# Performance work log

Measured on AMD Instinct MI355X. Metric: run time of the kernel, lower is better.

The kernel has to match this reference:

```python
import jax, jax.numpy as jnp
import numpy as np

NUM_HEADS = 4
GROUPS = 8
EPS = 1e-5


def setup_inputs() -> dict:
    key = jax.random.key(0)
    ks = jax.random.split(key, 8)
    B, C, H, W = 8, 512, 64, 64
    L, E = 77, 768
    std = 0.02
    return {
        "x": jax.random.normal(ks[0], (B, C, H, W), jnp.float32),
        "text_emb": jax.random.normal(ks[1], (B, L, E), jnp.float32),
        "attention_mask": jax.random.randint(ks[2], (B, L), 0, 2, jnp.int32),
        "Wq_w": jax.random.normal(ks[3], (C, C), jnp.float32) * std,
        "Wq_b": jnp.zeros((C,), jnp.float32),
        "Wk_w": jax.random.normal(ks[4], (C, E), jnp.float32) * std,
        "Wk_b": jnp.zeros((C,), jnp.float32),
        "Wv_w": jax.random.normal(ks[5], (C, E), jnp.float32) * std,
        "Wv_b": jnp.zeros((C,), jnp.float32),
        "gn_scale": jnp.ones((C,), jnp.float32),
        "gn_bias": jnp.zeros((C,), jnp.float32),
    }


def reference(x, text_emb, attention_mask, Wq_w, Wq_b, Wk_w, Wk_b, Wv_w, Wv_b, gn_scale, gn_bias):
    B, C, H, W = x.shape
    dh = C // NUM_HEADS
    scale = dh ** -0.5

    # [B, HW, C] queries from image features
    x_flat = x.reshape(B, C, H * W).transpose(0, 2, 1)
    Q = x_flat @ Wq_w.T + Wq_b                 # [B, S, C]
    K = text_emb @ Wk_w.T + Wk_b               # [B, L, C]
    V = text_emb @ Wv_w.T + Wv_b               # [B, L, C]

    def split_heads(t):
        Bt, T, _ = t.shape
        return t.reshape(Bt, T, NUM_HEADS, dh).transpose(0, 2, 1, 3)  # [B, h, T, dh]

    Qh, Kh, Vh = split_heads(Q), split_heads(K), split_heads(V)

    scores = jnp.einsum("bhqd,bhkd->bhqk", Qh, Kh) * scale  # [B, h, S, L]
    mask = (attention_mask == 0)[:, None, None, :]
    scores = jnp.where(mask, -jnp.inf, scores)
    probs = jax.nn.softmax(scores, axis=-1)
    # dropout layers are identity in eval mode
    attn = jnp.einsum("bhqk,bhkd->bhqd", probs, Vh)          # [B, h, S, dh]

    out = attn.transpose(0, 2, 1, 3).reshape(B, H * W, C)    # [B, S, C]
    out = out.transpose(0, 2, 1).reshape(B, C, H, W)

    # GroupNorm(8 groups, affine) over (C/G, H, W) per group
    g = out.reshape(B, GROUPS, -1)
    mean = g.mean(axis=-1, keepdims=True)
    var = g.var(axis=-1, keepdims=True)
    g = (g - mean) * jax.lax.rsqrt(var + EPS)
    out = g.reshape(B, C, H, W) * gn_scale[None, :, None, None] + gn_bias[None, :, None, None]
    return out
```

## Files before the change

### kernel.cpp

```cpp
#include <hip/hip_runtime.h>
#include <hip/hip_bf16.h>
#include <cstdint>


typedef __attribute__((ext_vector_type(8))) short short8;
typedef __attribute__((ext_vector_type(4))) short short4v;
typedef __attribute__((ext_vector_type(4))) float f32x4;

#define DEV __device__ __forceinline__

DEV float bf2f(unsigned short u){ union{uint32_t i; float f;} x; x.i = ((uint32_t)u) << 16; return x.f; }
DEV unsigned short f2bf(float f){ __hip_bfloat16 h = __float2bfloat16(f); return *reinterpret_cast<unsigned short*>(&h); }
DEV short8 ld8(const unsigned short* p){ return *reinterpret_cast<const short8*>(p); }
DEV f32x4 ldf4(const float* p){ return *reinterpret_cast<const f32x4*>(p); }

#if defined(__has_builtin)
#if __has_builtin(__builtin_amdgcn_global_load_lds)
#define HAVE_ASYNC_LDS 1
#endif
#endif

__global__ __launch_bounds__(256) void k_fat(const float* __restrict__ x,
                                             unsigned short* __restrict__ xTt,
                                             const float* __restrict__ text,
                                             const float* __restrict__ Wk,
                                             const float* __restrict__ Wkb,
                                             const float* __restrict__ Wv,
                                             const float* __restrict__ Wvb,
                                             unsigned short* __restrict__ wsK,
                                             unsigned short* __restrict__ wsVt,
                                             const float* __restrict__ Wq,
                                             unsigned short* __restrict__ wsWqT,
                                             int b0, int s_base, int slen, int SB){
  __shared__ unsigned short U[16896];
  const int tid = threadIdx.x;
  const int bx = blockIdx.x, by = blockIdx.y, bz = blockIdx.z;
  const int bg = b0 + bz;

  if (bx >= 3){
    const int cc = by, c0 = cc * 64;
    const int tile = bx - 3;
    const int s0 = s_base + tile * 256;
    {
      const int r = tid >> 2, sub = tid & 3;
      const float* src = &x[((size_t)(bg * 512 + c0 + r)) * 4096 + s0 + sub * 64];
      f32x4 rv[16];
      #pragma unroll
      for (int i = 0; i < 16; ++i) rv[i] = ldf4(src + i * 4);
      unsigned short* drow = &U[r * 264 + sub * 64];
      #pragma unroll
      for (int i = 0; i < 8; ++i){
        short8 v;
        #pragma unroll
        for (int j = 0; j < 4; ++j){ v[j] = (short)f2bf(rv[2*i][j]); v[j + 4] = (short)f2bf(rv[2*i+1][j]); }
        *reinterpret_cast<short8*>(drow + i * 8) = v;
      }
    }
    __syncthreads();
    {
      const int j = tid;
      unsigned short v[64];
      #pragma unroll
      for (int r = 0; r < 64; ++r) v[r] = U[r * 264 + j];
      const int sloc = tile * 256 + j;
      unsigned short* dst = &xTt[(((size_t)bz * 8 + cc) * slen + sloc) * 64];
      #pragma unroll
      for (int g = 0; g < 8; ++g)
        *reinterpret_cast<short8*>(dst + g * 8) = *reinterpret_cast<short8*>(&v[g * 8]);
    }
  } else if (bx < 2){
    unsigned short* At = U;
    unsigned short* Bt = U + 5760;
    const int wave = tid >> 6, lane = tid & 63;
    const int m16 = lane & 15, quad = lane >> 4;
    const int uc = bx * 8 + by;
    const int u0 = uc * 64;
    const bool isK = (u0 < 512);
    const float* W  = isK ? Wk  : Wv;
    const float* Wb = isK ? Wkb : Wvb;
    const int c0 = u0 & 511;
    const int c  = c0 + wave * 16 + m16;

    int srow[9], se4[9]; bool sA[9], sval[9];
    #pragma unroll
    for (int it = 0; it < 9; ++it){
      int slot = tid + it * 256;
      if (slot < 1280){ sA[it] = true;  srow[it] = slot >> 4;          se4[it] = (slot & 15) * 4; sval[it] = (srow[it] < 77); }
      else            { sA[it] = false; srow[it] = (slot - 1280) >> 4; se4[it] = ((slot - 1280) & 15) * 4; sval[it] = true; }
    }
    f32x4 preg[9];
    auto issue = [&](int kc){
      const int e0 = kc * 64;
      #pragma unroll
      for (int it = 0; it < 9; ++it){
        if (sA[it])
          preg[it] = sval[it] ? ldf4(&text[((size_t)(bg * 77 + srow[it])) * 768 + e0 + se4[it]])
                              : (f32x4){0.f, 0.f, 0.f, 0.f};
        else
          preg[it] = ldf4(&W[((size_t)(c0 + srow[it])) * 768 + e0 + se4[it]]);
      }
    };
    auto write_lds = [&](){
      #pragma unroll
      for (int it = 0; it < 9; ++it){
        short4v o;
        #pragma unroll
        for (int j = 0; j < 4; ++j) o[j] = (short)f2bf(preg[it][j]);
        if (sA[it]) *reinterpret_cast<short4v*>(&At[srow[it] * 72 + se4[it]]) = o;
        else        *reinterpret_cast<short4v*>(&Bt[srow[it] * 72 + se4[it]]) = o;
      }
    };

    f32x4 acc[5];
    #pragma unroll
    for (int mt = 0; mt < 5; ++mt) acc[mt] = (f32x4){0.f, 0.f, 0.f, 0.f};
    issue(0);
    for (int kc = 0; kc < 12; ++kc){
      write_lds();
      __syncthreads();
      if (kc < 11) issue(kc + 1);
      #pragma unroll
      for (int kk = 0; kk < 64; kk += 32){
        short8 bf_ = *reinterpret_cast<const short8*>(&Bt[(wave * 16 + m16) * 72 + kk + quad * 8]);
        #pragma unroll
        for (int mt = 0; mt < 5; ++mt){
          short8 af_ = *reinterpret_cast<const short8*>(&At[(mt * 16 + m16) * 72 + kk + quad * 8]);
          acc[mt] = __builtin_amdgcn_mfma_f32_16x16x32_bf16(af_, bf_, acc[mt], 0, 0, 0);
        }
      }
      __syncthreads();
    }
    const float bias = Wb[c];
    if (isK){
      #pragma unroll
      for (int mt = 0; mt < 5; ++mt)
        #pragma unroll
        for (int r = 0; r < 4; ++r){
          int l = mt * 16 + quad * 4 + r;
          if (l < 77) wsK[((size_t)(bz * 77 + l)) * 512 + c] = f2bf(acc[mt][r] + bias);
        }
    } else {
      unsigned short* vr = &wsVt[((size_t)(bz * 512 + c)) * 96];
      #pragma unroll
      for (int mt = 0; mt < 5; ++mt){
        short4v pk;
        #pragma unroll
        for (int r = 0; r < 4; ++r) pk[r] = (short)f2bf(acc[mt][r] + bias);
        *reinterpret_cast<short4v*>(&vr[mt * 16 + quad * 4]) = pk;
      }
      short4v z = {};
      *reinterpret_cast<short4v*>(&vr[80 + quad * 4]) = z;
    }
  } else {
    unsigned short* t = U;
    const int nb = 8 * SB;
    const int p  = by + bz * 8;
    for (int tile = p; tile < 64; tile += nb){
      const int ti = tile >> 3, tj = tile & 7;
      {
        const int r = tid >> 2, sub = tid & 3;
        const float* src = &Wq[((size_t)(tj * 64 + r)) * 512 + ti * 64 + sub * 16];
        f32x4 rv[4];
        #pragma unroll
        for (int i = 0; i < 4; ++i) rv[i] = ldf4(src + i * 4);
        unsigned short* drow = &t[r * 72 + sub * 16];
        #pragma unroll
        for (int i = 0; i < 2; ++i){
          short8 v;
          #pragma unroll
          for (int j = 0; j < 4; ++j){ v[j] = (short)f2bf(rv[2*i][j]); v[j + 4] = (short)f2bf(rv[2*i+1][j]); }
          *reinterpret_cast<short8*>(drow + i * 8) = v;
        }
      }
      __syncthreads();
      #pragma unroll
      for (int it = 0; it < 2; ++it){
        int slot = tid + it * 256;
        int j = slot >> 3, i8 = slot & 7;
        short8 v;
        #pragma unroll
        for (int q = 0; q < 8; ++q)
          v[q] = (short)t[(i8 * 8 + q) * 72 + (j & 63)];
        *reinterpret_cast<short8*>(&wsWqT[((size_t)(ti * 64 + j)) * 512 + tj * 64 + i8 * 8]) = v;
      }
      __syncthreads();
    }
  }
}

__global__ __launch_bounds__(256) void k1b(const unsigned short* __restrict__ wsWqT,
                                           const unsigned short* __restrict__ wsK,
                                           const float* __restrict__ Wqb,
                                           unsigned short* __restrict__ wsKWq,
                                           float* __restrict__ kbias){
  const int tid = threadIdx.x;
  const int wave = tid >> 6, lane = tid & 63;
  const int m16 = lane & 15, quad = lane >> 4;
  const int cq = blockIdx.x, h = blockIdx.y, bz = blockIdx.z;
  const int cbase = cq * 128 + wave * 32;

  f32x4 acc[2][5];
  #pragma unroll
  for (int mt = 0; mt < 2; ++mt)
    #pragma unroll
    for (int nt = 0; nt < 5; ++nt) acc[mt][nt] = (f32x4){0.f, 0.f, 0.f, 0.f};

  #pragma unroll
  for (int ks = 0; ks < 4; ++ks){
    short8 aw[2];
    #pragma unroll
    for (int mt = 0; mt < 2; ++mt)
      aw[mt] = ld8(&wsWqT[(size_t)(cbase + mt * 16 + m16) * 512 + h * 128 + ks * 32 + quad * 8]);
    #pragma unroll
    for (int nt = 0; nt < 5; ++nt){
      int l = nt * 16 + m16;
      short8 bk = {};
      if (l < 77) bk = ld8(&wsK[((size_t)(bz * 77 + l)) * 512 + h * 128 + ks * 32 + quad * 8]);
      #pragma unroll
      for (int mt = 0; mt < 2; ++mt)
        acc[mt][nt] = __builtin_amdgcn_mfma_f32_16x16x32_bf16(aw[mt], bk, acc[mt][nt], 0, 0, 0);
    }
  }
  #pragma unroll
  for (int mt = 0; mt < 2; ++mt)
    #pragma unroll
    for (int nt = 0; nt < 5; ++nt){
      int l = nt * 16 + m16;
      short4v pk;
      #pragma unroll
      for (int r = 0; r < 4; ++r) pk[r] = (short)f2bf(acc[mt][nt][r]);
      *reinterpret_cast<short4v*>(&wsKWq[((size_t)((bz * 4 + h) * 80 + l)) * 512 + cbase + mt * 16 + quad * 4]) = pk;
    }
  if (cq == 0 && tid < 80){
    int l = tid;
    float kb = 0.f;
    if (l < 77){
      #pragma unroll
      for (int d = 0; d < 128; d += 8){
        short8 kv = ld8(&wsK[((size_t)(bz * 77 + l)) * 512 + h * 128 + d]);
        f32x4 wa = ldf4(&Wqb[h * 128 + d]);
        f32x4 wb = ldf4(&Wqb[h * 128 + d + 4]);
        #pragma unroll
        for (int j = 0; j < 4; ++j){
          kb += bf2f((unsigned short)kv[j]) * wa[j];
          kb += bf2f((unsigned short)kv[j + 4]) * wb[j];
        }
      }
    }
    kbias[(bz * 4 + h) * 80 + l] = kb;
  }
}

__global__ __launch_bounds__(256, 4) void k2_attn(const unsigned short* __restrict__ xTt,
                                                  const unsigned short* __restrict__ wsKWq,
                                                  const unsigned short* __restrict__ wsVt,
                                                  const int* __restrict__ amask,
                                                  const float* __restrict__ kbias,
                                                  float* __restrict__ out,
                                                  float* __restrict__ gnacc,
                                                  int b0, int s_base, int slen){
  __shared__ unsigned short arena[13312];
  __shared__ float maskf[96];
  unsigned short* Pt = arena;

  const int tid = threadIdx.x;
  const int wave = tid >> 6, lane = tid & 63;
  const int m16 = lane & 15, quad = lane >> 4;
  const int bz = blockIdx.x, h = blockIdx.y, st = blockIdx.z;
  const int bg = b0 + bz;
  const int s_glob = s_base + st * 128;
  const int R0 = (wave >> 1) * 64, C0 = (wave & 1) * 64;
  const int sw0 = wave * 32;
  const float scale = 0.08838834764831845f;

  if (tid < 96){
    int l = tid;
    float mbv = -30000.f;
    if (l < 77 && amask[bg * 77 + l] != 0) mbv = kbias[(bz * 4 + h) * 80 + l] * scale;
    maskf[l] = mbv;
  }

  const unsigned short* Abase = wsKWq + (size_t)((bz * 4 + h) * 80) * 512;
  const unsigned short* Bb    = xTt + (size_t)(bz * 8) * slen * 64;
  const int srow0 = st * 128 + sw0;

  f32x4 acc2[5][2];
  #pragma unroll
  for (int mt = 0; mt < 5; ++mt){ acc2[mt][0] = (f32x4){0.f,0.f,0.f,0.f}; acc2[mt][1] = (f32x4){0.f,0.f,0.f,0.f}; }

  auto stageA = [&](int kc, int buf){
    const int sbase = buf * 5120;
    #pragma unroll
    for (int it = 0; it < 3; ++it){
      const int ubase = it * 256 + wave * 64;
      if (ubase < 640){
        const int u = ubase + lane;
        int l = u >> 3, pos = (u & 7) ^ (l & 7);
        const unsigned short* src = Abase + (size_t)l * 512 + kc * 64 + pos * 8;
#ifdef HAVE_ASYNC_LDS
        __builtin_amdgcn_global_load_lds((const __attribute__((address_space(1))) void*)src,
                                         (__attribute__((address_space(3))) void*)&arena[sbase + ubase * 8],
                                         16, 0, 0);
#else
        *reinterpret_cast<short8*>(&arena[sbase + u * 8]) = ld8(src);
#endif
      }
    }
  };

  short8 Breg[2][4];
  auto loadB = [&](int kc, int buf){
    const unsigned short* Bc = Bb + ((size_t)kc * slen + srow0) * 64;
    #pragma unroll
    for (int nt = 0; nt < 2; ++nt)
      #pragma unroll
      for (int kk = 0; kk < 2; ++kk)
        Breg[buf][nt * 2 + kk] = ld8(&Bc[(size_t)(nt * 16 + m16) * 64 + kk * 32 + quad * 8]);
  };

  auto compute = [&](int buf){
    const int ab = buf * 5120;
    #pragma unroll
    for (int kk = 0; kk < 2; ++kk){
      short8 af[5];
      #pragma unroll
      for (int mt = 0; mt < 5; ++mt){
        int l = mt * 16 + m16;
        int p = (kk * 4 + quad) ^ (l & 7);
        af[mt] = *reinterpret_cast<const short8*>(&arena[ab + l * 64 + p * 8]);
      }
      #pragma unroll
      for (int mt = 0; mt < 5; ++mt)
        #pragma unroll
        for (int nt = 0; nt < 2; ++nt)
          acc2[mt][nt] = __builtin_amdgcn_mfma_f32_16x16x32_bf16(af[mt], Breg[buf][nt * 2 + kk], acc2[mt][nt], 0, 0, 0);
    }
  };

  stageA(0, 0);
  loadB(0, 0);
  __syncthreads();
  #pragma unroll
  for (int kc = 0; kc < 8; ++kc){
    if (kc < 7){ stageA(kc + 1, (kc + 1) & 1); loadB(kc + 1, (kc + 1) & 1); }
    compute(kc & 1);
    __syncthreads();
  }

  const unsigned short* Vb = wsVt + (size_t)(bz * 512 + h * 128) * 96;
  short8 av0[4];
  #pragma unroll
  for (int mt = 0; mt < 4; ++mt)
    av0[mt] = ld8(&Vb[(size_t)(R0 + mt * 16 + m16) * 96 + quad * 8]);

  {
    float mb[5][4];
    #pragma unroll
    for (int mt = 0; mt < 5; ++mt)
      #pragma unroll
      for (int r = 0; r < 4; ++r) mb[mt][r] = maskf[mt * 16 + quad * 4 + r];
    #pragma unroll
    for (int nt = 0; nt < 2; ++nt){
      float sv[5][4]; float mx = -3e38f;
      #pragma unroll
      for (int mt = 0; mt < 5; ++mt)
        #pragma unroll
        for (int r = 0; r < 4; ++r){
          float v = acc2[mt][nt][r] * scale + mb[mt][r];
          sv[mt][r] = v; mx = fmaxf(mx, v);
        }
      mx = fmaxf(mx, __shfl_xor(mx, 16)); mx = fmaxf(mx, __shfl_xor(mx, 32));
      float sum = 0.f;
      #pragma unroll
      for (int mt = 0; mt < 5; ++mt)
        #pragma unroll
        for (int r = 0; r < 4; ++r){ float e = __expf(sv[mt][r] - mx); sv[mt][r] = e; sum += e; }
      sum += __shfl_xor(sum, 16); sum += __shfl_xor(sum, 32);
      float inv = 1.0f / sum;
      int sl = sw0 + nt * 16 + m16;
      #pragma unroll
      for (int mt = 0; mt < 5; ++mt){
        short4v pk;
        #pragma unroll
        for (int r = 0; r < 4; ++r) pk[r] = (short)f2bf(sv[mt][r] * inv);
        *reinterpret_cast<short4v*>(&Pt[sl * 104 + mt * 16 + quad * 4]) = pk;
      }
      short4v z = {};
      *reinterpret_cast<short4v*>(&Pt[sl * 104 + 80 + quad * 4]) = z;
    }
  }
  __syncthreads();

  f32x4 acc3[4][4];
  #pragma unroll
  for (int mt = 0; mt < 4; ++mt)
    #pragma unroll
    for (int nt = 0; nt < 4; ++nt) acc3[mt][nt] = (f32x4){0.f, 0.f, 0.f, 0.f};
  #pragma unroll
  for (int ks = 0; ks < 3; ++ks){
    short8 av[4], bp[4];
    #pragma unroll
    for (int mt = 0; mt < 4; ++mt)
      av[mt] = (ks == 0) ? av0[mt]
                         : ld8(&Vb[(size_t)(R0 + mt * 16 + m16) * 96 + ks * 32 + quad * 8]);
    #pragma unroll
    for (int nt = 0; nt < 4; ++nt)
      bp[nt] = *reinterpret_cast<const short8*>(&Pt[(C0 + nt * 16 + m16) * 104 + ks * 32 + quad * 8]);
    #pragma unroll
    for (int mt = 0; mt < 4; ++mt)
      #pragma unroll
      for (int nt = 0; nt < 4; ++nt)
        acc3[mt][nt] = __builtin_amdgcn_mfma_f32_16x16x32_bf16(av[mt], bp[nt], acc3[mt][nt], 0, 0, 0);
  }
  float sum = 0.f, ssq = 0.f;
  #pragma unroll
  for (int mt = 0; mt < 4; ++mt)
    #pragma unroll
    for (int nt = 0; nt < 4; ++nt){
      int sidx = s_glob + C0 + nt * 16 + m16;
      #pragma unroll
      for (int r = 0; r < 4; ++r){
        float v = acc3[mt][nt][r];
        sum += v; ssq += v * v;
        int d = h * 128 + R0 + mt * 16 + quad * 4 + r;
        out[(size_t)(bg * 512 + d) * 4096 + sidx] = v;
      }
    }
  #pragma unroll
  for (int off = 1; off < 64; off <<= 1){ sum += __shfl_xor(sum, off); ssq += __shfl_xor(ssq, off); }
  if (lane == 0){
    int g = h * 2 + (R0 >> 6);
    atomicAdd(&gnacc[(bg * 8 + g) * 2],     sum);
    atomicAdd(&gnacc[(bg * 8 + g) * 2 + 1], ssq);
  }
}

__global__ __launch_bounds__(256) void k3_gn(float* __restrict__ out,
                                             const float* __restrict__ gnacc,
                                             const float* __restrict__ gns,
                                             const float* __restrict__ gnb){
  const int bx = blockIdx.x;
  const int b = bx >> 9, c = bx & 511;
  const int g = c >> 6;
  const float s  = gnacc[(b * 8 + g) * 2];
  const float ss = gnacc[(b * 8 + g) * 2 + 1];
  const float invN = 1.f / 262144.f;
  const float mean = s * invN;
  const float var  = ss * invN - mean * mean;
  const float rstd = rsqrtf(fmaxf(var, 0.f) + 1e-5f);
  const float a  = rstd * gns[c];
  const float bb = gnb[c] - mean * a;
  const size_t base = (size_t)bx * 4096;
  #pragma unroll
  for (int p = 0; p < 4; ++p){
    size_t off = base + p * 1024 + threadIdx.x * 4;
    f32x4 v = ldf4(&out[off]);
    f32x4 o;
    #pragma unroll
    for (int j = 0; j < 4; ++j) o[j] = v[j] * a + bb;
    *reinterpret_cast<f32x4*>(&out[off]) = o;
  }
}

extern "C" void kernel_launch(void* const* d_in, const int* in_sizes, int n_in,
                              void* d_out, int out_size, void* d_ws, size_t ws_size,
                              hipStream_t stream){
  (void)in_sizes; (void)n_in; (void)out_size;
  const float* x    = (const float*)d_in[0];
  const float* text = (const float*)d_in[1];
  const int*   am   = (const int*)d_in[2];
  const float* Wq   = (const float*)d_in[3];
  const float* Wqb  = (const float*)d_in[4];
  const float* Wk   = (const float*)d_in[5];
  const float* Wkb  = (const float*)d_in[6];
  const float* Wv   = (const float*)d_in[7];
  const float* Wvb  = (const float*)d_in[8];
  const float* gns  = (const float*)d_in[9];
  const float* gnb  = (const float*)d_in[10];
  float* out = (float*)d_out;

  auto need = [](int SB, int SLEN) -> size_t {
    return 512ull + 524288ull + (size_t)SB * 506112ull + (size_t)SB * SLEN * 1024ull;
  };
  int SB = 8, SLEN = 4096;
  if      (ws_size >= need(8, 4096)) { SB = 8; SLEN = 4096; }
  else if (ws_size >= need(4, 4096)) { SB = 4; SLEN = 4096; }
  else if (ws_size >= need(2, 4096)) { SB = 2; SLEN = 4096; }
  else if (ws_size >= need(1, 4096)) { SB = 1; SLEN = 4096; }
  else if (ws_size >= need(1, 1024)) { SB = 1; SLEN = 1024; }
  else                               { SB = 1; SLEN = 256;  }

  uint8_t* ws = (uint8_t*)d_ws;
  float*          gnacc = (float*)ws;
  unsigned short* wsWqT = (unsigned short*)(ws + 512);
  unsigned short* wsK   = wsWqT + 512 * 512;
  unsigned short* wsVt  = wsK  + (size_t)SB * 77 * 512;
  unsigned short* wsKWq = wsVt + (size_t)SB * 512 * 96;
  float*          kbias = (float*)(wsKWq + (size_t)SB * 4 * 80 * 512);
  unsigned short* xTt   = (unsigned short*)(kbias + (size_t)SB * 4 * 80);

  hipMemsetAsync(gnacc, 0, 128 * sizeof(float), stream);
  for (int b0 = 0; b0 < 8; b0 += SB){
    for (int s_base = 0; s_base < 4096; s_base += SLEN){
      const int NT = SLEN >> 8;
      k_fat<<<dim3(NT + 3, 8, SB), 256, 0, stream>>>(x, xTt, text, Wk, Wkb, Wv, Wvb,
                                                     wsK, wsVt, Wq, wsWqT, b0, s_base, SLEN, SB);
      if (s_base == 0)
        k1b<<<dim3(4, 4, SB), 256, 0, stream>>>(wsWqT, wsK, Wqb, wsKWq, kbias);
      k2_attn<<<dim3(SB, 4, SLEN / 128), 256, 0, stream>>>(xTt, wsKWq, wsVt, am, kbias,
                                                           out, gnacc, b0, s_base, SLEN);
    }
  }
  k3_gn<<<4096, 256, 0, stream>>>(out, gnacc, gns, gnb);
}
```

Before: 117.9 us.

## Stage attention output as bf16 via LDS transpose before GroupNorm pass

```diff
diff --git a/kernel.cpp b/kernel.cpp
--- a/kernel.cpp
+++ b/kernel.cpp
@@ -257,8 +257,9 @@
                                                   const int* __restrict__ amask,
                                                   const float* __restrict__ kbias,
                                                   float* __restrict__ out,
+                                                  unsigned short* __restrict__ outTmp,
                                                   float* __restrict__ gnacc,
-                                                  int b0, int s_base, int slen){
+                                                  int b0, int s_base, int slen, int useTmp){
   __shared__ unsigned short arena[13312];
   __shared__ float maskf[96];
   unsigned short* Pt = arena;
@@ -412,26 +413,102 @@
       for (int nt = 0; nt < 4; ++nt)
         acc3[mt][nt] = __builtin_amdgcn_mfma_f32_16x16x32_bf16(av[mt], bp[nt], acc3[mt][nt], 0, 0, 0);
   }
+
   float sum = 0.f, ssq = 0.f;
   #pragma unroll
   for (int mt = 0; mt < 4; ++mt)
     #pragma unroll
-    for (int nt = 0; nt < 4; ++nt){
-      int sidx = s_glob + C0 + nt * 16 + m16;
+    for (int nt = 0; nt < 4; ++nt)
       #pragma unroll
       for (int r = 0; r < 4; ++r){
         float v = acc3[mt][nt][r];
         sum += v; ssq += v * v;
-        int d = h * 128 + R0 + mt * 16 + quad * 4 + r;
-        out[(size_t)(bg * 512 + d) * 4096 + sidx] = v;
-      }
-    }
+      }
   #pragma unroll
   for (int off = 1; off < 64; off <<= 1){ sum += __shfl_xor(sum, off); ssq += __shfl_xor(ssq, off); }
   if (lane == 0){
     int g = h * 2 + (R0 >> 6);
     atomicAdd(&gnacc[(bg * 8 + g) * 2],     sum);
     atomicAdd(&gnacc[(bg * 8 + g) * 2 + 1], ssq);
+  }
+
+  if (useTmp){
+    __syncthreads();
+    float* T = reinterpret_cast<float*>(arena);
+    const int TS = 132;
+    #pragma unroll
+    for (int p = 0; p < 4; ++p){
+      if ((R0 >> 6) == (p >> 1)){
+        #pragma unroll
+        for (int mt2 = 0; mt2 < 2; ++mt2){
+          int mt = (p & 1) * 2 + mt2;
+          #pragma unroll
+          for (int nt = 0; nt < 4; ++nt)
+            #pragma unroll
+            for (int r = 0; r < 4; ++r)
+              T[(mt2 * 16 + quad * 4 + r) * TS + C0 + nt * 16 + m16] = acc3[mt][nt][r];
+        }
+      }
+      __syncthreads();
+      #pragma unroll
+      for (int it = 0; it < 4; ++it){
+        int row = wave * 8 + it * 2 + (lane >> 5);
+        int c = h * 128 + p * 32 + row;
+        int sc = (lane & 31) * 4;
+        f32x4 v = *reinterpret_cast<const f32x4*>(&T[row * TS + sc]);
+        short4v o;
+        #pragma unroll
+        for (int j = 0; j < 4; ++j) o[j] = (short)f2bf(v[j]);
+        *reinterpret_cast<short4v*>(&outTmp[(size_t)(bg * 512 + c) * 4096 + s_glob + sc]) = o;
+      }
+      __syncthreads();
+    }
+  } else {
+    #pragma unroll
+    for (int mt = 0; mt < 4; ++mt)
+      #pragma unroll
+      for (int nt = 0; nt < 4; ++nt){
+        int sidx = s_glob + C0 + nt * 16 + m16;
+        #pragma unroll
+        for (int r = 0; r < 4; ++r){
+          int d = h * 128 + R0 + mt * 16 + quad * 4 + r;
+          out[(size_t)(bg * 512 + d) * 4096 + sidx] = acc3[mt][nt][r];
+        }
+      }
+  }
+}
+
+__global__ __launch_bounds__(256) void k3_gn_b(const unsigned short* __restrict__ tmp,
+                                               float* __restrict__ out,
+                                               const float* __restrict__ gnacc,
+                                               const float* __restrict__ gns,
+                                               const float* __restrict__ gnb){
+  const int bx = blockIdx.x;
+  const int b = bx >> 9, c = bx & 511;
+  const int g = c >> 6;
+  const float s  = gnacc[(b * 8 + g) * 2];
+  const float ss = gnacc[(b * 8 + g) * 2 + 1];
+  const float invN = 1.f / 262144.f;
+  const float mean = s * invN;
+  const float var  = ss * invN - mean * mean;
+  const float rstd = rsqrtf(fmaxf(var, 0.f) + 1e-5f);
+  const float a  = rstd * gns[c];
+  const float bb = gnb[c] - mean * a;
+  const size_t base = (size_t)bx * 4096;
+  const unsigned short* src = &tmp[base + threadIdx.x * 16];
+  float* dst = &out[base + threadIdx.x * 16];
+  short8 v0 = ld8(src), v1 = ld8(src + 8);
+  #pragma unroll
+  for (int k = 0; k < 2; ++k){
+    short8 v = k ? v1 : v0;
+    f32x4 o0, o1;
+    #pragma unroll
+    for (int j = 0; j < 4; ++j){
+      o0[j] = bf2f((unsigned short)v[j])     * a + bb;
+      o1[j] = bf2f((unsigned short)v[j + 4]) * a + bb;
+    }
+    *reinterpret_cast<f32x4*>(dst + k * 8)     = o0;
+    *reinterpret_cast<f32x4*>(dst + k * 8 + 4) = o1;
   }
 }
 
@@ -490,6 +567,9 @@
   else if (ws_size >= need(1, 1024)) { SB = 1; SLEN = 1024; }
   else                               { SB = 1; SLEN = 256;  }
 
+  const size_t tmpBytes = 8ull * 512 * 4096 * 2;
+  const int useTmp = (SB == 8 && SLEN == 4096 && ws_size >= need(8, 4096) + tmpBytes) ? 1 : 0;
+
   uint8_t* ws = (uint8_t*)d_ws;
   float*          gnacc = (float*)ws;
   unsigned short* wsWqT = (unsigned short*)(ws + 512);
@@ -498,6 +578,7 @@
   unsigned short* wsKWq = wsVt + (size_t)SB * 512 * 96;
   float*          kbias = (float*)(wsKWq + (size_t)SB * 4 * 80 * 512);
   unsigned short* xTt   = (unsigned short*)(kbias + (size_t)SB * 4 * 80);
+  unsigned short* outTmp = xTt + (size_t)SB * 8 * SLEN * 64;
 
   hipMemsetAsync(gnacc, 0, 128 * sizeof(float), stream);
   for (int b0 = 0; b0 < 8; b0 += SB){
@@ -508,8 +589,12 @@
       if (s_base == 0)
         k1b<<<dim3(4, 4, SB), 256, 0, stream>>>(wsWqT, wsK, Wqb, wsKWq, kbias);
       k2_attn<<<dim3(SB, 4, SLEN / 128), 256, 0, stream>>>(xTt, wsKWq, wsVt, am, kbias,
-                                                           out, gnacc, b0, s_base, SLEN);
-    }
-  }
-  k3_gn<<<4096, 256, 0, stream>>>(out, gnacc, gns, gnb);
+                                                           out, outTmp, gnacc,
+                                                           b0, s_base, SLEN, useTmp);
+    }
+  }
+  if (useTmp)
+    k3_gn_b<<<4096, 256, 0, stream>>>(outTmp, out, gnacc, gns, gnb);
+  else
+    k3_gn<<<4096, 256, 0, stream>>>(out, gnacc, gns, gnb);
 }
```

Result: slower. 121.1 us (+2.7%).
